# Kernel optimization log

Hardware: AMD Instinct MI355X
Metric: run time of the kernel (lower is better)

Reference implementation:

```python
import jax, jax.numpy as jnp
import numpy as np

H, KV, D = 16, 4, 128
WIN = 512
EPS = 1e-6


def rms_norm(x, w):
    # x: [..., D]
    return x * jax.lax.rsqrt(jnp.mean(x * x, axis=-1, keepdims=True) + EPS) * w


def rotate_half(x):
    x1, x2 = jnp.split(x, 2, axis=-1)
    return jnp.concatenate([-x2, x1], axis=-1)


def setup_inputs() -> dict:
    key = jax.random.key(0)
    ks = jax.random.split(key, 8)
    B, L, hidden = 2, 2048, 2048
    x = jax.random.normal(ks[0], (B, L, hidden), jnp.float32)
    # realistic RoPE tables
    inv_freq = 1.0 / (10000.0 ** (np.arange(0, D, 2, dtype=np.float32) / D))
    t = np.arange(L, dtype=np.float32)
    freqs = np.outer(t, inv_freq)  # [L, D/2]
    emb = np.concatenate([freqs, freqs], axis=-1)  # [L, D]
    cos = jnp.asarray(np.cos(emb), jnp.float32)
    sin = jnp.asarray(np.sin(emb), jnp.float32)
    s = 0.02
    Wq = jax.random.normal(ks[1], (H * D, hidden), jnp.float32) * s
    Wk = jax.random.normal(ks[2], (KV * D, hidden), jnp.float32) * s
    Wv = jax.random.normal(ks[3], (KV * D, hidden), jnp.float32) * s
    Wo = jax.random.normal(ks[4], (hidden, H * D), jnp.float32) * s
    q_norm_w = jnp.ones((D,), jnp.float32)
    k_norm_w = jnp.ones((D,), jnp.float32)
    return {"x": x, "cos": cos, "sin": sin, "Wq": Wq, "Wk": Wk, "Wv": Wv,
            "Wo": Wo, "q_norm_w": q_norm_w, "k_norm_w": k_norm_w}


def reference(x, cos, sin, Wq, Wk, Wv, Wo, q_norm_w, k_norm_w):
    B, L, _ = x.shape
    # projections (torch Linear: y = x @ W.T)
    q = (x @ Wq.T).reshape(B, L, H, D)
    k = (x @ Wk.T).reshape(B, L, KV, D)
    v = (x @ Wv.T).reshape(B, L, KV, D)
    # QK RMSNorm, then [B, heads, L, D]
    q = jnp.transpose(rms_norm(q, q_norm_w), (0, 2, 1, 3))
    k = jnp.transpose(rms_norm(k, k_norm_w), (0, 2, 1, 3))
    v = jnp.transpose(v, (0, 2, 1, 3))
    # RoPE
    c = cos[None, None]  # [1,1,L,D]
    s = sin[None, None]
    q = q * c + rotate_half(q) * s
    k = k * c + rotate_half(k) * s
    # GQA repeat_interleave over head dim
    n_rep = H // KV
    k = jnp.repeat(k, n_rep, axis=1)
    v = jnp.repeat(v, n_rep, axis=1)
    # sliding-window additive bias [L, L]
    idx = jnp.arange(L)
    in_win = jnp.abs(idx[:, None] - idx[None, :]) <= WIN
    bias = jnp.where(in_win, 0.0, jnp.finfo(x.dtype).min).astype(x.dtype)
    # SDPA
    scale = 1.0 / jnp.sqrt(jnp.asarray(D, x.dtype))
    scores = jnp.einsum('bhqd,bhkd->bhqk', q, k) * scale + bias[None, None]
    attn = jax.nn.softmax(scores, axis=-1)
    out = jnp.einsum('bhqk,bhkd->bhqd', attn, v)  # [B,H,L,D]
    out = jnp.transpose(out, (0, 2, 1, 3)).reshape(B, L, H * D)
    return out @ Wo.T
```

## Files before the change

kernel.cpp:

```cpp
#include <hip/hip_runtime.h>
#include <hip/hip_bf16.h>


typedef unsigned short u16;
typedef unsigned int u32;
typedef __attribute__((ext_vector_type(8))) short bf16x8;
typedef __attribute__((ext_vector_type(4))) float f32x4;

#define AS1 __attribute__((address_space(1)))
#define AS3 __attribute__((address_space(3)))

__device__ __forceinline__ u16 f2b(float f) {
  union { float f; u32 u; } c; c.f = f;
  return (u16)((c.u + 0x8000u) >> 16);
}
__device__ __forceinline__ float b2f(u16 u) {
  union { u32 u; float f; } c; c.u = ((u32)u) << 16; return c.f;
}

__global__ __launch_bounds__(256) void cvt_all(const float* __restrict__ x,
                                               const float* __restrict__ wq,
                                               const float* __restrict__ wk,
                                               const float* __restrict__ wv,
                                               const float* __restrict__ wo,
                                               u16* __restrict__ xb,
                                               u16* __restrict__ wqkvb,
                                               u16* __restrict__ wob) {
  int blk = blockIdx.x;
  const float* s; u16* d; int off;
  if (blk < 8192)       { s = x;  d = xb;              off = blk * 1024; }
  else if (blk < 12288) { s = wq; d = wqkvb;           off = (blk - 8192) * 1024; }
  else if (blk < 13312) { s = wk; d = wqkvb + 4194304; off = (blk - 12288) * 1024; }
  else if (blk < 14336) { s = wv; d = wqkvb + 5242880; off = (blk - 13312) * 1024; }
  else                  { s = wo; d = wob;             off = (blk - 14336) * 1024; }
  int i = off + threadIdx.x * 4;
  float4 v = *(const float4*)(s + i);
  ushort4 o;
  o.x = f2b(v.x); o.y = f2b(v.y); o.z = f2b(v.z); o.w = f2b(v.w);
  *(ushort4*)(d + i) = o;
}

template<int F32OUT>
__global__ __launch_bounds__(256) void gemm_bt(const u16* __restrict__ A,
                                               const u16* __restrict__ Bm,
                                               void* __restrict__ C,
                                               int M, int N, int K) {
  __shared__ u16 As[128][64];
  __shared__ u16 Bs[128][64];
  const int tid  = threadIdx.x;
  const int w    = tid >> 6, lane = tid & 63, quad = lane >> 4, l16 = lane & 15;
  const int wm   = w >> 1, wn = w & 1;
  const int m0   = blockIdx.y * 128, n0 = blockIdx.x * 128;

  f32x4 zero = {0.f, 0.f, 0.f, 0.f};
  f32x4 acc[4][4];
#pragma unroll
  for (int i = 0; i < 4; i++)
#pragma unroll
    for (int j = 0; j < 4; j++) acc[i][j] = zero;

  const int srow = lane >> 3;
  const int swz8 = ((lane & 7) ^ (lane >> 3)) * 8;

  for (int k0 = 0; k0 < K; k0 += 64) {
#pragma unroll
    for (int p = 0; p < 4; ++p) {
      int row = p * 32 + w * 8 + srow;
      __builtin_amdgcn_global_load_lds(
          (const AS1 void*)(A + (size_t)(m0 + row) * K + k0 + swz8),
          (AS3 void*)((char*)&As[0][0] + p * 4096 + w * 1024), 16, 0, 0);
      __builtin_amdgcn_global_load_lds(
          (const AS1 void*)(Bm + (size_t)(n0 + row) * K + k0 + swz8),
          (AS3 void*)((char*)&Bs[0][0] + p * 4096 + w * 1024), 16, 0, 0);
    }
    __syncthreads();
#pragma unroll
    for (int kk = 0; kk < 64; kk += 32) {
      const int cs = ((kk >> 3) + quad) ^ (l16 & 7);
      bf16x8 af[4], bfr[4];
#pragma unroll
      for (int i = 0; i < 4; i++)
        af[i] = *(const bf16x8*)((const char*)&As[0][0] +
                                 (wm * 64 + i * 16 + l16) * 128 + cs * 16);
#pragma unroll
      for (int j = 0; j < 4; j++)
        bfr[j] = *(const bf16x8*)((const char*)&Bs[0][0] +
                                  (wn * 64 + j * 16 + l16) * 128 + cs * 16);
#pragma unroll
      for (int i = 0; i < 4; i++)
#pragma unroll
        for (int j = 0; j < 4; j++)
          acc[i][j] = __builtin_amdgcn_mfma_f32_16x16x32_bf16(af[i], bfr[j], acc[i][j], 0, 0, 0);
    }
    __syncthreads();
  }

#pragma unroll
  for (int i = 0; i < 4; i++) {
#pragma unroll
    for (int r = 0; r < 4; r++) {
      int gr = m0 + wm * 64 + i * 16 + quad * 4 + r;
#pragma unroll
      for (int j = 0; j < 4; j++) {
        int gc = n0 + wn * 64 + j * 16 + l16;
        if (F32OUT) ((float*)C)[(size_t)gr * N + gc] = acc[i][j][r];
        else        ((u16*)C)[(size_t)gr * N + gc]   = f2b(acc[i][j][r]);
      }
    }
  }
}

__global__ __launch_bounds__(256) void rmsrope_tv(const u16* __restrict__ qkv,
                                                  const float* __restrict__ cosT,
                                                  const float* __restrict__ sinT,
                                                  const float* __restrict__ qw,
                                                  const float* __restrict__ kw,
                                                  u16* __restrict__ qo,
                                                  u16* __restrict__ ko,
                                                  u16* __restrict__ vt) {
  __shared__ u16 T[64][72];
  if (blockIdx.x < 20480) {
    int wid  = blockIdx.x * 4 + (threadIdx.x >> 6);
    int lane = threadIdx.x & 63;
    int r  = wid / 20;
    int hh = wid % 20;
    int b = r >> 11, l = r & 2047;
    int cb = hh < 16 ? hh * 128 : 2048 + (hh - 16) * 128;
    const u16* src = qkv + (size_t)r * 3072 + cb;
    float v0 = b2f(src[lane]);
    float v1 = b2f(src[lane + 64]);
    float ss = v0 * v0 + v1 * v1;
#pragma unroll
    for (int off = 1; off < 64; off <<= 1) ss += __shfl_xor(ss, off, 64);
    float inv = rsqrtf(ss * (1.0f / 128.0f) + 1e-6f);
    const float* wt = hh < 16 ? qw : kw;
    float n0 = v0 * inv * wt[lane];
    float n1 = v1 * inv * wt[lane + 64];
    float c0 = cosT[l * 128 + lane],      c1 = cosT[l * 128 + 64 + lane];
    float s0 = sinT[l * 128 + lane],      s1 = sinT[l * 128 + 64 + lane];
    float o0 = n0 * c0 - n1 * s0;
    float o1 = n1 * c1 + n0 * s1;
    const float qscale = 0.08838834764831845f * 1.4426950408889634f;
    u16* dst; size_t base;
    if (hh < 16) { dst = qo; base = ((size_t)(b * 16 + hh) * 2048 + l) * 128;
                   o0 *= qscale; o1 *= qscale; }
    else         { dst = ko; base = ((size_t)(b * 4 + (hh - 16)) * 2048 + l) * 128; }
    dst[base + lane]      = f2b(o0);
    dst[base + 64 + lane] = f2b(o1);
  } else {
    int bid = blockIdx.x - 20480;
    const int lt = bid & 31, dt = (bid >> 5) & 1, bh = bid >> 6;
    const int b = bh >> 2, kv = bh & 3;
    const u16* s = qkv + ((size_t)(b * 2048 + lt * 64)) * 3072 + 2560 + kv * 128 + dt * 64;
    u16*       d = vt + (size_t)bh * 128 * 2048 + (size_t)dt * 64 * 2048 + lt * 64;
    const int t = threadIdx.x;
    const int row = t >> 3, c8 = (t & 7) * 8;
#pragma unroll
    for (int p = 0; p < 2; ++p)
      *(uint4*)&T[p * 32 + row][c8] = *(const uint4*)(s + (size_t)(p * 32 + row) * 3072 + c8);
    __syncthreads();
#pragma unroll
    for (int p = 0; p < 2; ++p) {
      int dr = p * 32 + row;
      u16 o[8];
#pragma unroll
      for (int j = 0; j < 8; ++j) o[j] = T[c8 + j][dr];
      *(uint4*)(d + (size_t)dr * 2048 + c8) = *(uint4*)o;
    }
  }
}

__global__ __launch_bounds__(512) void flash_swa(const u16* __restrict__ Q,
                                                 const u16* __restrict__ Kg,
                                                 const u16* __restrict__ VTg,
                                                 u16* __restrict__ Og) {
  constexpr int L = 2048, D = 128;
  __shared__ u16 Ks[2][64][128];
  __shared__ u16 Vt[2][128][64];
  __shared__ u16 Ps[8][32][72];

  const int flat = blockIdx.x;
  const int kvh  = flat & 3;
  const int b    = (flat >> 2) & 1;
  const int q0   = (flat >> 3) * 64;
  const int tid = threadIdx.x;
  const int w = tid >> 6, lane = tid & 63, quad = lane >> 4, l16 = lane & 15;
  const int hd = kvh * 4 + (w >> 1);
  const int qh = w & 1;

  const u16* Qb  = Q   + (size_t)(b * 16 + hd)  * L * D;
  const u16* Kb  = Kg  + (size_t)(b * 4 + kvh) * L * D;
  const u16* VTb = VTg + (size_t)(b * 4 + kvh) * D * L;

  bf16x8 qf[2][4];
#pragma unroll
  for (int qs = 0; qs < 2; ++qs) {
    int qr = q0 + qh * 32 + qs * 16 + l16;
#pragma unroll
    for (int ks = 0; ks < 4; ++ks)
      qf[qs][ks] = *(const bf16x8*)(Qb + (size_t)qr * D + ks * 32 + quad * 8);
  }
  const int qi0 = q0 + qh * 32 + l16;

  int kt0   = q0 > 512 ? q0 - 512 : 0;
  int ktend = q0 + 64 + 512; if (ktend > L) ktend = L;
  const int nt = (ktend - kt0) >> 6;

  const u16* srcK[2];
  const u16* srcV[2];
#pragma unroll
  for (int j = 0; j < 2; ++j) {
    int rk = w * 8 + j * 4 + quad;
    int ck = ((lane & 15) ^ (rk & 7)) * 8;
    srcK[j] = Kb + (size_t)(kt0 + rk) * D + ck;
    int rv = w * 16 + j * 8 + (lane >> 3);
    int cv = ((lane & 7) ^ ((lane >> 3) & 7)) * 8;
    srcV[j] = VTb + (size_t)rv * L + kt0 + cv;
  }

#define STAGE(bb) do {                                                        \
    char* kdst = (char*)&Ks[bb][0][0] + w * 2048;                             \
    char* vdst = (char*)&Vt[bb][0][0] + w * 2048;                             \
    _Pragma("unroll")                                                         \
    for (int j = 0; j < 2; ++j) {                                             \
      __builtin_amdgcn_global_load_lds((const AS1 void*)srcK[j],              \
          (AS3 void*)(kdst + j * 1024), 16, 0, 0);                            \
      srcK[j] += 64 * D;                                                      \
    }                                                                         \
    _Pragma("unroll")                                                         \
    for (int j = 0; j < 2; ++j) {                                             \
      __builtin_amdgcn_global_load_lds((const AS1 void*)srcV[j],              \
          (AS3 void*)(vdst + j * 1024), 16, 0, 0);                            \
      srcV[j] += 64;                                                          \
    }                                                                         \
  } while (0)

  f32x4 zero = {0.f, 0.f, 0.f, 0.f};
  f32x4 o[2][8];
#pragma unroll
  for (int qs = 0; qs < 2; ++qs)
#pragma unroll
    for (int i = 0; i < 8; i++) o[qs][i] = zero;
  float lrow[2] = {0.f, 0.f};

  STAGE(0);
  __syncthreads();
  int cur = 0;

  for (int t = 0; t < nt; ++t) {
    const int kt = kt0 + t * 64;
    if (t + 1 < nt) STAGE(cur ^ 1);

    const char* kbase = (const char*)&Ks[cur][0][0];
    const char* vbase = (const char*)&Vt[cur][0][0];

    f32x4 s[2][4];
#pragma unroll
    for (int qs = 0; qs < 2; ++qs)
#pragma unroll
      for (int ct = 0; ct < 4; ct++) s[qs][ct] = zero;
    __builtin_amdgcn_s_setprio(1);
#pragma unroll
    for (int ks = 0; ks < 4; ++ks) {
#pragma unroll
      for (int ct = 0; ct < 4; ++ct) {
        bf16x8 kf = *(const bf16x8*)(kbase + (ct * 16 + l16) * 256 +
                                     (((ks * 4 + quad) ^ (l16 & 7)) * 16));
        s[0][ct] = __builtin_amdgcn_mfma_f32_16x16x32_bf16(kf, qf[0][ks], s[0][ct], 0, 0, 0);
        s[1][ct] = __builtin_amdgcn_mfma_f32_16x16x32_bf16(kf, qf[1][ks], s[1][ct], 0, 0, 0);
      }
    }
    __builtin_amdgcn_s_setprio(0);

    bool need_mask = (kt + 448 < q0) || (kt > q0 + 448);
#pragma unroll
    for (int qs = 0; qs < 2; ++qs) {
      float psum = 0.f;
      u16* psw = &Ps[w][qs * 16 + l16][0];
#pragma unroll
      for (int ct = 0; ct < 4; ct++) {
        u16 ph[4];
#pragma unroll
        for (int r = 0; r < 4; r++) {
          float x = s[qs][ct][r];
          if (need_mask) {
            int ki = kt + ct * 16 + quad * 4 + r;
            int dd = (qi0 + qs * 16) - ki; if (dd < 0) dd = -dd;
            if (dd > 512) x = -__builtin_inff();
          }
          float p = exp2f(x);
          psum += p;
          ph[r] = f2b(p);
        }
        uint2 pk;
        pk.x = (u32)ph[0] | ((u32)ph[1] << 16);
        pk.y = (u32)ph[2] | ((u32)ph[3] << 16);
        *(uint2*)(psw + ct * 16 + quad * 4) = pk;
      }
      psum += __shfl_xor(psum, 16, 64);
      psum += __shfl_xor(psum, 32, 64);
      lrow[qs] += psum;
    }

    bf16x8 pf[2][2];
#pragma unroll
    for (int qs = 0; qs < 2; ++qs) {
#pragma unroll
      for (int ks2 = 0; ks2 < 2; ++ks2)
        pf[qs][ks2] = *(const bf16x8*)(&Ps[w][qs * 16 + l16][ks2 * 32 + quad * 8]);
    }
    __builtin_amdgcn_s_setprio(1);
#pragma unroll
    for (int dt = 0; dt < 8; ++dt) {
#pragma unroll
      for (int ks2 = 0; ks2 < 2; ++ks2) {
        bf16x8 vf = *(const bf16x8*)(vbase + (dt * 16 + l16) * 128 +
                                     (((ks2 * 4 + quad) ^ (l16 & 7)) * 16));
        o[0][dt] = __builtin_amdgcn_mfma_f32_16x16x32_bf16(pf[0][ks2], vf, o[0][dt], 0, 0, 0);
        o[1][dt] = __builtin_amdgcn_mfma_f32_16x16x32_bf16(pf[1][ks2], vf, o[1][dt], 0, 0, 0);
      }
    }
    __builtin_amdgcn_s_setprio(0);

    __syncthreads();
    cur ^= 1;
  }
#undef STAGE

#pragma unroll
  for (int qs = 0; qs < 2; ++qs) {
#pragma unroll
    for (int r = 0; r < 4; r++) {
      float lv  = __shfl(lrow[qs], (lane & 48) + quad * 4 + r, 64);
      float inv = 1.0f / lv;
      int qr = q0 + qh * 32 + qs * 16 + quad * 4 + r;
      size_t base = ((size_t)(b * L + qr)) * 2048 + hd * 128;
#pragma unroll
      for (int dt = 0; dt < 8; dt++)
        Og[base + dt * 16 + l16] = f2b(o[qs][dt][r] * inv);
    }
  }
}

extern "C" void kernel_launch(void* const* d_in, const int* in_sizes, int n_in,
                              void* d_out, int out_size, void* d_ws, size_t ws_size,
                              hipStream_t stream) {
  const float* x    = (const float*)d_in[0];
  const float* cosT = (const float*)d_in[1];
  const float* sinT = (const float*)d_in[2];
  const float* Wq   = (const float*)d_in[3];
  const float* Wk   = (const float*)d_in[4];
  const float* Wv   = (const float*)d_in[5];
  const float* Wo   = (const float*)d_in[6];
  const float* qw   = (const float*)d_in[7];
  const float* kw   = (const float*)d_in[8];

  char* ws = (char*)d_ws;
  u16* x_bf    = (u16*)(ws + 0);
  u16* wqkv_bf = (u16*)(ws + 16777216);
  u16* wo_bf   = (u16*)(ws + 29360128);
  u16* qkv_bf  = (u16*)(ws + 37748736);
  u16* q_bf    = (u16*)(ws + 62914560);
  u16* k_bf    = (u16*)(ws + 79691776);
  u16* vt_bf   = wqkv_bf;
  u16* attn_bf = x_bf;

  cvt_all<<<18432, 256, 0, stream>>>(x, Wq, Wk, Wv, Wo, x_bf, wqkv_bf, wo_bf);
  gemm_bt<0><<<dim3(24, 32), 256, 0, stream>>>(x_bf, wqkv_bf, qkv_bf, 4096, 3072, 2048);
  rmsrope_tv<<<20992, 256, 0, stream>>>(qkv_bf, cosT, sinT, qw, kw, q_bf, k_bf, vt_bf);
  flash_swa<<<dim3(256, 1, 1), 512, 0, stream>>>(q_bf, k_bf, vt_bf, attn_bf);
  gemm_bt<1><<<dim3(16, 32), 256, 0, stream>>>(attn_bf, wo_bf, d_out, 4096, 2048, 2048);
}
```

Baseline: 312.5 us.

## Fuse QK RMSNorm, RoPE and V transpose into QKV GEMM epilogue

The QKV projection GEMM now applies RMSNorm, RoPE and the query scale directly in its epilogue, and writes V already transposed. This removes the separate rmsrope_tv kernel and the bf16 qkv intermediate buffer round trip. Each 128-column tile maps to one head, and the B-fragment column mapping is remapped so each wave holds the d and d+64 pairs RoPE needs. Row sums of squares are reduced across the two wn waves through shared memory. The cost is a heavier epilogue with scattered cos/sin loads and 2-byte stores, plus an extra barrier.

```diff
diff --git a/kernel.cpp b/kernel.cpp
--- a/kernel.cpp
+++ b/kernel.cpp
@@ -40,17 +40,24 @@
   *(ushort4*)(d + i) = o;
 }
 
-template<int F32OUT>
-__global__ __launch_bounds__(256) void gemm_bt(const u16* __restrict__ A,
-                                               const u16* __restrict__ Bm,
-                                               void* __restrict__ C,
-                                               int M, int N, int K) {
+__global__ __launch_bounds__(256) void gemm_qkv(const u16* __restrict__ A,
+                                                const u16* __restrict__ Bm,
+                                                const float* __restrict__ cosT,
+                                                const float* __restrict__ sinT,
+                                                const float* __restrict__ qw,
+                                                const float* __restrict__ kw,
+                                                u16* __restrict__ qo,
+                                                u16* __restrict__ ko,
+                                                u16* __restrict__ vt) {
+  constexpr int K = 2048;
   __shared__ u16 As[128][64];
   __shared__ u16 Bs[128][64];
+  __shared__ float Rs[2][2][64];
   const int tid  = threadIdx.x;
   const int w    = tid >> 6, lane = tid & 63, quad = lane >> 4, l16 = lane & 15;
   const int wm   = w >> 1, wn = w & 1;
-  const int m0   = blockIdx.y * 128, n0 = blockIdx.x * 128;
+  const int m0   = blockIdx.y * 128;
+  const int hh   = blockIdx.x;
 
   f32x4 zero = {0.f, 0.f, 0.f, 0.f};
   f32x4 acc[4][4];
@@ -61,6 +68,7 @@
 
   const int srow = lane >> 3;
   const int swz8 = ((lane & 7) ^ (lane >> 3)) * 8;
+  const int n0   = hh * 128;
 
   for (int k0 = 0; k0 < K; k0 += 64) {
 #pragma unroll
@@ -85,7 +93,7 @@
 #pragma unroll
       for (int j = 0; j < 4; j++)
         bfr[j] = *(const bf16x8*)((const char*)&Bs[0][0] +
-                                  (wn * 64 + j * 16 + l16) * 128 + cs * 16);
+                                  (wn * 32 + (j & 1) * 16 + (j >> 1) * 64 + l16) * 128 + cs * 16);
 #pragma unroll
       for (int i = 0; i < 4; i++)
 #pragma unroll
@@ -95,6 +103,138 @@
     __syncthreads();
   }
 
+  const int bidx = m0 >> 11;
+  const int lbase = (m0 & 2047) + wm * 64;
+
+  if (hh < 20) {
+    float ssq[4][4];
+#pragma unroll
+    for (int i = 0; i < 4; i++)
+#pragma unroll
+      for (int r = 0; r < 4; r++) {
+        float s2 = acc[i][0][r] * acc[i][0][r] + acc[i][1][r] * acc[i][1][r] +
+                   acc[i][2][r] * acc[i][2][r] + acc[i][3][r] * acc[i][3][r];
+#pragma unroll
+        for (int m = 1; m < 16; m <<= 1) s2 += __shfl_xor(s2, m, 64);
+        ssq[i][r] = s2;
+      }
+    if (l16 == 0) {
+#pragma unroll
+      for (int i = 0; i < 4; i++)
+#pragma unroll
+        for (int r = 0; r < 4; r++)
+          Rs[wm][wn][i * 16 + quad * 4 + r] = ssq[i][r];
+    }
+    __syncthreads();
+
+    float inv[4][4];
+#pragma unroll
+    for (int i = 0; i < 4; i++)
+#pragma unroll
+      for (int r = 0; r < 4; r++) {
+        int row64 = i * 16 + quad * 4 + r;
+        float sum = Rs[wm][0][row64] + Rs[wm][1][row64];
+        inv[i][r] = rsqrtf(sum * (1.0f / 128.0f) + 1e-6f);
+      }
+
+    const float* wt = hh < 16 ? qw : kw;
+    const float qs_ = hh < 16 ? 0.08838834764831845f * 1.4426950408889634f : 1.0f;
+    u16* dst; size_t hb;
+    if (hh < 16) { dst = qo; hb = (size_t)(bidx * 16 + hh) * 2048 * 128; }
+    else         { dst = ko; hb = (size_t)(bidx * 4 + (hh - 16)) * 2048 * 128; }
+
+#pragma unroll
+    for (int j = 0; j < 2; ++j) {
+      const int d = wn * 32 + j * 16 + l16;
+      const float wtd = wt[d], wtdp = wt[d + 64];
+#pragma unroll
+      for (int i = 0; i < 4; i++) {
+#pragma unroll
+        for (int r = 0; r < 4; r++) {
+          int l = lbase + i * 16 + quad * 4 + r;
+          float nv0 = acc[i][j][r]     * inv[i][r] * wtd;
+          float nv1 = acc[i][j + 2][r] * inv[i][r] * wtdp;
+          float c0 = cosT[l * 128 + d],      s0v = sinT[l * 128 + d];
+          float c1 = cosT[l * 128 + d + 64], s1v = sinT[l * 128 + d + 64];
+          float o0 = (nv0 * c0 - nv1 * s0v) * qs_;
+          float o1 = (nv1 * c1 + nv0 * s1v) * qs_;
+          dst[hb + (size_t)l * 128 + d]      = f2b(o0);
+          dst[hb + (size_t)l * 128 + d + 64] = f2b(o1);
+        }
+      }
+    }
+  } else {
+    const int kv = hh - 20;
+    u16* dv = vt + (size_t)(bidx * 4 + kv) * 128 * 2048;
+#pragma unroll
+    for (int i = 0; i < 4; i++) {
+      int l0 = lbase + i * 16 + quad * 4;
+#pragma unroll
+      for (int j = 0; j < 4; j++) {
+        int d = wn * 32 + (j & 1) * 16 + (j >> 1) * 64 + l16;
+        u16 p[4];
+#pragma unroll
+        for (int r = 0; r < 4; r++) p[r] = f2b(acc[i][j][r]);
+        *(uint2*)(dv + (size_t)d * 2048 + l0) = *(uint2*)p;
+      }
+    }
+  }
+}
+
+__global__ __launch_bounds__(256) void gemm_bt(const u16* __restrict__ A,
+                                               const u16* __restrict__ Bm,
+                                               float* __restrict__ C,
+                                               int M, int N, int K) {
+  __shared__ u16 As[128][64];
+  __shared__ u16 Bs[128][64];
+  const int tid  = threadIdx.x;
+  const int w    = tid >> 6, lane = tid & 63, quad = lane >> 4, l16 = lane & 15;
+  const int wm   = w >> 1, wn = w & 1;
+  const int m0   = blockIdx.y * 128, n0 = blockIdx.x * 128;
+
+  f32x4 zero = {0.f, 0.f, 0.f, 0.f};
+  f32x4 acc[4][4];
+#pragma unroll
+  for (int i = 0; i < 4; i++)
+#pragma unroll
+    for (int j = 0; j < 4; j++) acc[i][j] = zero;
+
+  const int srow = lane >> 3;
+  const int swz8 = ((lane & 7) ^ (lane >> 3)) * 8;
+
+  for (int k0 = 0; k0 < K; k0 += 64) {
+#pragma unroll
+    for (int p = 0; p < 4; ++p) {
+      int row = p * 32 + w * 8 + srow;
+      __builtin_amdgcn_global_load_lds(
+          (const AS1 void*)(A + (size_t)(m0 + row) * K + k0 + swz8),
+          (AS3 void*)((char*)&As[0][0] + p * 4096 + w * 1024), 16, 0, 0);
+      __builtin_amdgcn_global_load_lds(
+          (const AS1 void*)(Bm + (size_t)(n0 + row) * K + k0 + swz8),
+          (AS3 void*)((char*)&Bs[0][0] + p * 4096 + w * 1024), 16, 0, 0);
+    }
+    __syncthreads();
+#pragma unroll
+    for (int kk = 0; kk < 64; kk += 32) {
+      const int cs = ((kk >> 3) + quad) ^ (l16 & 7);
+      bf16x8 af[4], bfr[4];
+#pragma unroll
+      for (int i = 0; i < 4; i++)
+        af[i] = *(const bf16x8*)((const char*)&As[0][0] +
+                                 (wm * 64 + i * 16 + l16) * 128 + cs * 16);
+#pragma unroll
+      for (int j = 0; j < 4; j++)
+        bfr[j] = *(const bf16x8*)((const char*)&Bs[0][0] +
+                                  (wn * 64 + j * 16 + l16) * 128 + cs * 16);
+#pragma unroll
+      for (int i = 0; i < 4; i++)
+#pragma unroll
+        for (int j = 0; j < 4; j++)
+          acc[i][j] = __builtin_amdgcn_mfma_f32_16x16x32_bf16(af[i], bfr[j], acc[i][j], 0, 0, 0);
+    }
+    __syncthreads();
+  }
+
 #pragma unroll
   for (int i = 0; i < 4; i++) {
 #pragma unroll
@@ -103,69 +243,8 @@
 #pragma unroll
       for (int j = 0; j < 4; j++) {
         int gc = n0 + wn * 64 + j * 16 + l16;
-        if (F32OUT) ((float*)C)[(size_t)gr * N + gc] = acc[i][j][r];
-        else        ((u16*)C)[(size_t)gr * N + gc]   = f2b(acc[i][j][r]);
-      }
-    }
-  }
-}
-
-__global__ __launch_bounds__(256) void rmsrope_tv(const u16* __restrict__ qkv,
-                                                  const float* __restrict__ cosT,
-                                                  const float* __restrict__ sinT,
-                                                  const float* __restrict__ qw,
-                                                  const float* __restrict__ kw,
-                                                  u16* __restrict__ qo,
-                                                  u16* __restrict__ ko,
-                                                  u16* __restrict__ vt) {
-  __shared__ u16 T[64][72];
-  if (blockIdx.x < 20480) {
-    int wid  = blockIdx.x * 4 + (threadIdx.x >> 6);
-    int lane = threadIdx.x & 63;
-    int r  = wid / 20;
-    int hh = wid % 20;
-    int b = r >> 11, l = r & 2047;
-    int cb = hh < 16 ? hh * 128 : 2048 + (hh - 16) * 128;
-    const u16* src = qkv + (size_t)r * 3072 + cb;
-    float v0 = b2f(src[lane]);
-    float v1 = b2f(src[lane + 64]);
-    float ss = v0 * v0 + v1 * v1;
-#pragma unroll
-    for (int off = 1; off < 64; off <<= 1) ss += __shfl_xor(ss, off, 64);
-    float inv = rsqrtf(ss * (1.0f / 128.0f) + 1e-6f);
-    const float* wt = hh < 16 ? qw : kw;
-    float n0 = v0 * inv * wt[lane];
-    float n1 = v1 * inv * wt[lane + 64];
-    float c0 = cosT[l * 128 + lane],      c1 = cosT[l * 128 + 64 + lane];
-    float s0 = sinT[l * 128 + lane],      s1 = sinT[l * 128 + 64 + lane];
-    float o0 = n0 * c0 - n1 * s0;
-    float o1 = n1 * c1 + n0 * s1;
-    const float qscale = 0.08838834764831845f * 1.4426950408889634f;
-    u16* dst; size_t base;
-    if (hh < 16) { dst = qo; base = ((size_t)(b * 16 + hh) * 2048 + l) * 128;
-                   o0 *= qscale; o1 *= qscale; }
-    else         { dst = ko; base = ((size_t)(b * 4 + (hh - 16)) * 2048 + l) * 128; }
-    dst[base + lane]      = f2b(o0);
-    dst[base + 64 + lane] = f2b(o1);
-  } else {
-    int bid = blockIdx.x - 20480;
-    const int lt = bid & 31, dt = (bid >> 5) & 1, bh = bid >> 6;
-    const int b = bh >> 2, kv = bh & 3;
-    const u16* s = qkv + ((size_t)(b * 2048 + lt * 64)) * 3072 + 2560 + kv * 128 + dt * 64;
-    u16*       d = vt + (size_t)bh * 128 * 2048 + (size_t)dt * 64 * 2048 + lt * 64;
-    const int t = threadIdx.x;
-    const int row = t >> 3, c8 = (t & 7) * 8;
-#pragma unroll
-    for (int p = 0; p < 2; ++p)
-      *(uint4*)&T[p * 32 + row][c8] = *(const uint4*)(s + (size_t)(p * 32 + row) * 3072 + c8);
-    __syncthreads();
-#pragma unroll
-    for (int p = 0; p < 2; ++p) {
-      int dr = p * 32 + row;
-      u16 o[8];
-#pragma unroll
-      for (int j = 0; j < 8; ++j) o[j] = T[c8 + j][dr];
-      *(uint4*)(d + (size_t)dr * 2048 + c8) = *(uint4*)o;
+        C[(size_t)gr * N + gc] = acc[i][j][r];
+      }
     }
   }
 }
@@ -359,15 +438,15 @@
   u16* x_bf    = (u16*)(ws + 0);
   u16* wqkv_bf = (u16*)(ws + 16777216);
   u16* wo_bf   = (u16*)(ws + 29360128);
-  u16* qkv_bf  = (u16*)(ws + 37748736);
+  u16* vt_bf   = (u16*)(ws + 37748736);
   u16* q_bf    = (u16*)(ws + 62914560);
   u16* k_bf    = (u16*)(ws + 79691776);
-  u16* vt_bf   = wqkv_bf;
   u16* attn_bf = x_bf;
 
   cvt_all<<<18432, 256, 0, stream>>>(x, Wq, Wk, Wv, Wo, x_bf, wqkv_bf, wo_bf);
-  gemm_bt<0><<<dim3(24, 32), 256, 0, stream>>>(x_bf, wqkv_bf, qkv_bf, 4096, 3072, 2048);
-  rmsrope_tv<<<20992, 256, 0, stream>>>(qkv_bf, cosT, sinT, qw, kw, q_bf, k_bf, vt_bf);
+  gemm_qkv<<<dim3(24, 32), 256, 0, stream>>>(x_bf, wqkv_bf, cosT, sinT, qw, kw,
+                                             q_bf, k_bf, vt_bf);
   flash_swa<<<dim3(256, 1, 1), 512, 0, stream>>>(q_bf, k_bf, vt_bf, attn_bf);
-  gemm_bt<1><<<dim3(16, 32), 256, 0, stream>>>(attn_bf, wo_bf, d_out, 4096, 2048, 2048);
-}
+  gemm_bt<<<dim3(16, 32), 256, 0, stream>>>(attn_bf, wo_bf, (float*)d_out,
+                                            4096, 2048, 2048);
+}
```

Result: no change. 309.3 us (-1.0%).
